# Performance work log

Measured on AMD Instinct MI355X. Metric: run time of the kernel, lower is better.

Reference implementation:

```python
import jax, jax.numpy as jnp
import numpy as np

DIM = 1024
NUM_HEADS = 16
HEAD_DIM = DIM // NUM_HEADS
EPS = 1e-6


def setup_inputs() -> dict:
    key = jax.random.key(0)
    ks = jax.random.split(key, 12)
    B, S = 2, 2048
    scale = 0.02
    # rope angles -> cos/sin of shape [B, S, HEAD_DIM//2]
    inv_freq = 1.0 / (10000.0 ** (jnp.arange(0, HEAD_DIM, 2, dtype=jnp.float32) / HEAD_DIM))
    t = jnp.arange(S, dtype=jnp.float32)
    ang = jnp.einsum('s,d->sd', t, inv_freq)  # [S, HEAD_DIM//2]
    rope_cos = jnp.broadcast_to(jnp.cos(ang)[None], (B, S, HEAD_DIM // 2))
    rope_sin = jnp.broadcast_to(jnp.sin(ang)[None], (B, S, HEAD_DIM // 2))
    return {
        'hidden_states': jax.random.normal(ks[0], (B, S, DIM), dtype=jnp.float32),
        'rope_cos': rope_cos,
        'rope_sin': rope_sin,
        'Wq': jax.random.normal(ks[1], (DIM, DIM), dtype=jnp.float32) * scale,
        'bq': jnp.zeros((DIM,), jnp.float32),
        'Wk': jax.random.normal(ks[2], (DIM, DIM), dtype=jnp.float32) * scale,
        'bk': jnp.zeros((DIM,), jnp.float32),
        'Wv': jax.random.normal(ks[3], (DIM, DIM), dtype=jnp.float32) * scale,
        'bv': jnp.zeros((DIM,), jnp.float32),
        'q_norm_w': jnp.ones((HEAD_DIM,), jnp.float32),
        'k_norm_w': jnp.ones((HEAD_DIM,), jnp.float32),
        'Wo': jax.random.normal(ks[4], (DIM, DIM), dtype=jnp.float32) * scale,
        'bo': jnp.zeros((DIM,), jnp.float32),
    }


def _rms_norm(x, w):
    # FP32 RMSNorm over last dim (head_dim)
    x32 = x.astype(jnp.float32)
    inv = jax.lax.rsqrt(jnp.mean(x32 * x32, axis=-1, keepdims=True) + EPS)
    return (x32 * inv * w).astype(x.dtype)


def _apply_rope(x, cos, sin):
    # x: [B,H,S,D]; cos/sin: [B,S,D//2] -> broadcast over heads
    xr = x[..., 0::2]
    xi = x[..., 1::2]
    c = cos[:, None, :, :]
    s = sin[:, None, :, :]
    out_r = xr * c - xi * s
    out_i = xr * s + xi * c
    return jnp.stack([out_r, out_i], axis=-1).reshape(x.shape)


def reference(hidden_states, rope_cos, rope_sin, Wq, bq, Wk, bk, Wv, bv,
              q_norm_w, k_norm_w, Wo, bo):
    B, S, D = hidden_states.shape
    H, hd = NUM_HEADS, HEAD_DIM

    def proj(x, W, b):
        y = jnp.einsum('bsd,ed->bse', x, W) + b
        return y.reshape(B, S, H, hd).transpose(0, 2, 1, 3)  # [B,H,S,hd]

    q = proj(hidden_states, Wq, bq)
    k = proj(hidden_states, Wk, bk)
    v = proj(hidden_states, Wv, bv)

    q = _apply_rope(_rms_norm(q, q_norm_w), rope_cos, rope_sin)
    k = _apply_rope(_rms_norm(k, k_norm_w), rope_cos, rope_sin)

    scale = 1.0 / jnp.sqrt(jnp.asarray(hd, hidden_states.dtype))
    scores = jnp.einsum('bhqd,bhkd->bhqk', q, k) * scale
    attn = jax.nn.softmax(scores, axis=-1)
    o = jnp.einsum('bhqk,bhkd->bhqd', attn, v)  # [B,H,S,hd]
    o = o.transpose(0, 2, 1, 3).reshape(B, S, D)
    return jnp.einsum('bsd,ed->bse', o, Wo) + bo
```

## Files before the change

### kernel.cpp

```cpp
#include <hip/hip_runtime.h>
#include <math.h>

#define BATCH 2
#define SEQ 2048
#define D_MODEL 1024
#define NHEAD 16
#define HDIM 64
#define MROWS (BATCH * SEQ)
#define KDIM 1024

typedef __attribute__((ext_vector_type(8))) short bf16x8_t;
typedef __attribute__((ext_vector_type(4))) float f32x4_t;

#define KSCALE 0.18033688011112042f

__device__ __forceinline__ unsigned short f2bf(float x) {
    unsigned u = __builtin_bit_cast(unsigned, x);
    u += 0x7fffu + ((u >> 16) & 1u);
    return (unsigned short)(u >> 16);
}
__device__ __forceinline__ float bf2f(unsigned short h) {
    return __builtin_bit_cast(float, (unsigned)h << 16);
}
__device__ __forceinline__ unsigned cvt_pk_bf16(float lo, float hi) {
    unsigned r;
    asm("v_cvt_pk_bf16_f32 %0, %1, %2" : "=v"(r) : "v"(lo), "v"(hi));
    return r;
}
__device__ __forceinline__ float fexp2(float x) {
    float r;
    asm("v_exp_f32 %0, %1" : "=v"(r) : "v"(x));
    return r;
}

__device__ __forceinline__ void gload_lds16(const void* g, void* l) {
    __builtin_amdgcn_global_load_lds(
        (const __attribute__((address_space(1))) unsigned int*)g,
        (__attribute__((address_space(3))) unsigned int*)l, 16, 0, 0);
}

__global__ __launch_bounds__(256, 3) void gemm_qkv_bf16(
    const unsigned short* __restrict__ hbf,
    const unsigned short* __restrict__ wqb, const unsigned short* __restrict__ wkb,
    const unsigned short* __restrict__ wvb,
    const float* __restrict__ bq, const float* __restrict__ bk,
    const float* __restrict__ bv,
    const float* __restrict__ qw, const float* __restrict__ kw,
    const float* __restrict__ cosb, const float* __restrict__ sinb,
    unsigned short* __restrict__ qbf, unsigned short* __restrict__ kbf,
    unsigned short* __restrict__ vbf)
{
    __shared__ unsigned short lds[16384];
    const int bx = blockIdx.x;
    const int mat = bx >> 3;
    const int nc0 = (bx & 7) * 128;
    const int m0 = blockIdx.y * 128;
    const unsigned short* W = mat == 0 ? wqb : mat == 1 ? wkb : wvb;
    const float* bias = mat == 0 ? bq : mat == 1 ? bk : bv;

    const int tid = threadIdx.x;
    const int lane = tid & 63;
    const int w = tid >> 6;
    const int wm = w >> 1, wn = w & 1;
    const int l15 = lane & 15, lg = lane >> 4;
    const int r_in = lane >> 3, slot = lane & 7;

    f32x4_t acc[4][4];
    #pragma unroll
    for (int i = 0; i < 4; ++i)
        #pragma unroll
        for (int j = 0; j < 4; ++j) acc[i][j] = (f32x4_t){0.f, 0.f, 0.f, 0.f};

    const unsigned short* baseA = hbf + (size_t)m0 * KDIM;
    const unsigned short* baseW = W + (size_t)nc0 * KDIM;
    const int xk = (slot ^ r_in) << 3;

    for (int kt = 0; kt < 16; ++kt) {
        const int k = kt * 64;
        __syncthreads();
        #pragma unroll
        for (int cc = 0; cc < 8; ++cc) {
            const int row = ((((cc & 3) << 2) | w) << 3) + r_in;
            const unsigned short* src =
                (cc < 4 ? baseA : baseW) + (size_t)row * KDIM + k + xk;
            gload_lds16(src, &lds[(size_t)((cc << 2) | w) << 9]);
        }
        __syncthreads();

        #pragma unroll
        for (int ks = 0; ks < 2; ++ks) {
            bf16x8_t ah[4], wh[4];
            #pragma unroll
            for (int i = 0; i < 4; ++i) {
                const int r = wm * 64 + i * 16 + l15;
                const int off = r * 64 + ((((ks << 2) | lg) ^ (r & 7)) << 3);
                ah[i] = *(const bf16x8_t*)&lds[off];
            }
            #pragma unroll
            for (int j = 0; j < 4; ++j) {
                const int r = wn * 64 + j * 16 + l15;
                const int off = r * 64 + ((((ks << 2) | lg) ^ (r & 7)) << 3);
                wh[j] = *(const bf16x8_t*)&lds[8192 + off];
            }
            #pragma unroll
            for (int i = 0; i < 4; ++i)
                #pragma unroll
                for (int j = 0; j < 4; ++j)
                    acc[i][j] = __builtin_amdgcn_mfma_f32_16x16x32_bf16(ah[i], wh[j], acc[i][j], 0, 0, 0);
        }
    }

    if (mat == 2) {
        #pragma unroll
        for (int j = 0; j < 4; ++j) {
            const int n = nc0 + wn * 64 + j * 16 + l15;
            const float bb = bias[n];
            #pragma unroll
            for (int i = 0; i < 4; ++i)
                #pragma unroll
                for (int q = 0; q < 4; ++q) {
                    const int m = m0 + wm * 64 + i * 16 + lg * 4 + q;
                    vbf[(size_t)m * D_MODEL + n] = f2bf(acc[i][j][q] + bb);
                }
        }
    } else {
        unsigned short* dst = mat == 0 ? qbf : kbf;
        const float* nw = mat == 0 ? qw : kw;
        float bbj[4], wj[4];
        #pragma unroll
        for (int j = 0; j < 4; ++j) {
            bbj[j] = bias[nc0 + wn * 64 + j * 16 + l15];
            wj[j] = nw[j * 16 + l15];
        }
        const int headn = (nc0 + wn * 64) >> 6;
        #pragma unroll
        for (int i = 0; i < 4; ++i) {
            #pragma unroll
            for (int q = 0; q < 4; ++q) {
                const int m = m0 + wm * 64 + i * 16 + lg * 4 + q;
                float v[4];
                float ss = 0.0f;
                #pragma unroll
                for (int j = 0; j < 4; ++j) {
                    v[j] = acc[i][j][q] + bbj[j];
                    ss = fmaf(v[j], v[j], ss);
                }
                ss += __shfl_xor(ss, 1);
                ss += __shfl_xor(ss, 2);
                ss += __shfl_xor(ss, 4);
                ss += __shfl_xor(ss, 8);
                const float inv = rsqrtf(ss * (1.0f / 64.0f) + 1e-6f);
                const int bh = ((m >> 11) << 4) | headn;
                const size_t rowoff = (((size_t)bh << 11) | (size_t)(m & 2047)) << 6;
                #pragma unroll
                for (int j = 0; j < 4; ++j) {
                    float val = v[j] * inv * wj[j];
                    float partner = __shfl_xor(val, 1);
                    const int d = j * 16 + l15;
                    const float c = cosb[(size_t)m * (HDIM / 2) + (d >> 1)];
                    const float s = sinb[(size_t)m * (HDIM / 2) + (d >> 1)];
                    float outv = (l15 & 1) ? fmaf(partner, s, val * c)
                                           : fmaf(val, c, -partner * s);
                    if (mat) outv *= KSCALE;
                    dst[rowoff | d] = f2bf(outv);
                }
            }
        }
    }
}

__global__ __launch_bounds__(256, 2) void gemm_out(
    const unsigned short* __restrict__ ohi, const unsigned short* __restrict__ olo,
    const unsigned short* __restrict__ woh, const unsigned short* __restrict__ wol,
    const float* __restrict__ bo, float* __restrict__ out)
{
    __shared__ unsigned short lds[24576];
    const int nc0 = blockIdx.x * 64;
    const int m0 = blockIdx.y * 128;

    const int tid = threadIdx.x;
    const int lane = tid & 63;
    const int w = tid >> 6;
    const int l15 = lane & 15, lg = lane >> 4;
    const int r_in = lane >> 3, slot = lane & 7;

    f32x4_t acc[2][4];
    #pragma unroll
    for (int i = 0; i < 2; ++i)
        #pragma unroll
        for (int j = 0; j < 4; ++j) acc[i][j] = (f32x4_t){0.f, 0.f, 0.f, 0.f};

    const unsigned short* bA0 = ohi + (size_t)m0 * KDIM;
    const unsigned short* bA1 = olo + (size_t)m0 * KDIM;
    const unsigned short* bW0 = woh + (size_t)nc0 * KDIM;
    const unsigned short* bW1 = wol + (size_t)nc0 * KDIM;
    const int xk = (slot ^ r_in) << 3;

    for (int kt = 0; kt < 16; ++kt) {
        const int k = kt * 64;
        __syncthreads();
        #pragma unroll
        for (int cc = 0; cc < 12; ++cc) {
            const unsigned short* srcb;
            int row, base;
            if (cc < 4)       { srcb = bA0; row = cc * 32;        base = cc * 2048; }
            else if (cc < 8)  { srcb = bA1; row = (cc - 4) * 32;  base = 8192 + (cc - 4) * 2048; }
            else if (cc < 10) { srcb = bW0; row = (cc - 8) * 32;  base = 16384 + (cc - 8) * 2048; }
            else              { srcb = bW1; row = (cc - 10) * 32; base = 20480 + (cc - 10) * 2048; }
            row += w * 8 + r_in;
            gload_lds16(srcb + (size_t)row * KDIM + k + xk, &lds[base + w * 512]);
        }
        __syncthreads();

        #pragma unroll
        for (int ks = 0; ks < 2; ++ks) {
            bf16x8_t ah[2], al[2], wh[4], wl[4];
            #pragma unroll
            for (int i = 0; i < 2; ++i) {
                const int r = w * 32 + i * 16 + l15;
                const int off = r * 64 + ((((ks << 2) | lg) ^ (r & 7)) << 3);
                ah[i] = *(const bf16x8_t*)&lds[off];
                al[i] = *(const bf16x8_t*)&lds[8192 + off];
            }
            #pragma unroll
            for (int j = 0; j < 4; ++j) {
                const int r = j * 16 + l15;
                const int off = r * 64 + ((((ks << 2) | lg) ^ (r & 7)) << 3);
                wh[j] = *(const bf16x8_t*)&lds[16384 + off];
                wl[j] = *(const bf16x8_t*)&lds[20480 + off];
            }
            #pragma unroll
            for (int i = 0; i < 2; ++i)
                #pragma unroll
                for (int j = 0; j < 4; ++j) {
                    acc[i][j] = __builtin_amdgcn_mfma_f32_16x16x32_bf16(ah[i], wh[j], acc[i][j], 0, 0, 0);
                    acc[i][j] = __builtin_amdgcn_mfma_f32_16x16x32_bf16(ah[i], wl[j], acc[i][j], 0, 0, 0);
                    acc[i][j] = __builtin_amdgcn_mfma_f32_16x16x32_bf16(al[i], wh[j], acc[i][j], 0, 0, 0);
                }
        }
    }

    #pragma unroll
    for (int j = 0; j < 4; ++j) {
        const int n = nc0 + j * 16 + l15;
        const float bb = bo[n];
        #pragma unroll
        for (int i = 0; i < 2; ++i)
            #pragma unroll
            for (int q = 0; q < 4; ++q) {
                const int m = m0 + w * 32 + i * 16 + lg * 4 + q;
                out[(size_t)m * D_MODEL + n] = acc[i][j][q] + bb;
            }
    }
}

__global__ __launch_bounds__(256) void pack_all(
    const float* __restrict__ w0, const float* __restrict__ w1,
    const float* __restrict__ w2, const float* __restrict__ w3,
    const float* __restrict__ hsrc,
    unsigned short* __restrict__ b0, unsigned short* __restrict__ b1,
    unsigned short* __restrict__ b2,
    unsigned short* __restrict__ h3, unsigned short* __restrict__ l3,
    unsigned short* __restrict__ hdst)
{
    const int y = blockIdx.y;
    if (y < 3) {
        const float* src = y == 0 ? w0 : y == 1 ? w1 : w2;
        unsigned short* dst = y == 0 ? b0 : y == 1 ? b1 : b2;
        const int n4 = D_MODEL * D_MODEL / 4;
        for (int i = blockIdx.x * 256 + threadIdx.x; i < n4; i += gridDim.x * 256) {
            float4 v = ((const float4*)src)[i];
            ushort4 h;
            h.x = f2bf(v.x); h.y = f2bf(v.y); h.z = f2bf(v.z); h.w = f2bf(v.w);
            ((ushort4*)dst)[i] = h;
        }
    } else if (y == 3) {
        const int n4 = D_MODEL * D_MODEL / 4;
        for (int i = blockIdx.x * 256 + threadIdx.x; i < n4; i += gridDim.x * 256) {
            float4 v = ((const float4*)w3)[i];
            ushort4 h, l;
            h.x = f2bf(v.x); l.x = f2bf(v.x - bf2f(h.x));
            h.y = f2bf(v.y); l.y = f2bf(v.y - bf2f(h.y));
            h.z = f2bf(v.z); l.z = f2bf(v.z - bf2f(h.z));
            h.w = f2bf(v.w); l.w = f2bf(v.w - bf2f(h.w));
            ((ushort4*)h3)[i] = h;
            ((ushort4*)l3)[i] = l;
        }
    } else {
        const int n4 = MROWS * D_MODEL / 4;
        for (int i = blockIdx.x * 256 + threadIdx.x; i < n4; i += gridDim.x * 256) {
            float4 v = ((const float4*)hsrc)[i];
            ushort4 h;
            h.x = f2bf(v.x); h.y = f2bf(v.y); h.z = f2bf(v.z); h.w = f2bf(v.w);
            ((ushort4*)hdst)[i] = h;
        }
    }
}

__global__ __launch_bounds__(256) void vtrans_bf(
    const unsigned short* __restrict__ vbf, unsigned short* __restrict__ vbt)
{
    __shared__ unsigned short T[64][72];
    const int tid = threadIdx.x;
    const int bh = blockIdx.y;
    const int b = bh >> 4, h = bh & 15;
    const int s0 = blockIdx.x * 64;

    const int sr = tid >> 2;
    const int dc = (tid & 3) << 4;
    const unsigned short* src = vbf + ((size_t)b * SEQ + s0 + sr) * D_MODEL + h * HDIM + dc;
    unsigned short tmp[16];
    *(bf16x8_t*)tmp = *(const bf16x8_t*)src;
    *(bf16x8_t*)(tmp + 8) = *(const bf16x8_t*)(src + 8);
    #pragma unroll
    for (int i = 0; i < 16; ++i) T[dc + i][sr] = tmp[i];
    __syncthreads();

    const int dr = tid >> 2;
    const int sc = (tid & 3) << 4;
    unsigned short ov[16];
    #pragma unroll
    for (int i = 0; i < 16; ++i) ov[i] = T[dr][sc + i];
    unsigned short* dst = vbt + ((size_t)bh * HDIM + dr) * SEQ + s0 + sc;
    *(bf16x8_t*)dst = *(bf16x8_t*)ov;
    *(bf16x8_t*)(dst + 8) = *(bf16x8_t*)(ov + 8);
}

__global__ __launch_bounds__(256, 2) void attn_mfma(
    const unsigned short* __restrict__ qbf,
    const unsigned short* __restrict__ kbf,
    const unsigned short* __restrict__ vbt,
    unsigned short* __restrict__ ohi,
    unsigned short* __restrict__ olo)
{
    __shared__ __align__(16) char slds[49152];

    const int tid = threadIdx.x;
    const int lane = tid & 63;
    const int w = tid >> 6;
    const int l15 = lane & 15;
    const int lg = lane >> 4;
    const int e7 = l15 & 7;

    const int bh = blockIdx.y;
    const int q0 = blockIdx.x * 128;
    const int b = bh >> 4, h = bh & 15;

    bf16x8_t qa[2][2];
    #pragma unroll
    for (int g = 0; g < 2; ++g) {
        const size_t qrow = ((size_t)bh * SEQ + q0 + w * 32 + g * 16 + l15) * HDIM;
        qa[g][0] = *(const bf16x8_t*)&qbf[qrow + lg * 8];
        qa[g][1] = *(const bf16x8_t*)&qbf[qrow + 32 + lg * 8];
    }

    float lsum0 = 0.0f, lsum1 = 0.0f;
    f32x4_t oacc[2][4];
    #pragma unroll
    for (int g = 0; g < 2; ++g)
        #pragma unroll
        for (int db = 0; db < 4; ++db) oacc[g][db] = (f32x4_t){0.f, 0.f, 0.f, 0.f};

    const unsigned short* kt_base = kbf + (size_t)bh * SEQ * HDIM;
    const unsigned short* vt_base = vbt + (size_t)bh * HDIM * SEQ;

    const int lrow = (lane >> 3) & 7;
    const int lch = lane & 7;
    const unsigned short* kg0 = kt_base + (w * 16 + lrow) * HDIM + ((lch ^ lrow) << 3);
    const unsigned short* kg1 = kg0 + 8 * HDIM;
    const unsigned short* vg0 = vt_base + (size_t)(w * 16 + lrow) * SEQ + ((lch ^ lrow) << 3);
    const unsigned short* vg1 = vg0 + (size_t)8 * SEQ;

    char* const sK = slds;
    char* const sV = slds + 16384;
    char* const sP = slds + 32768;
    const int woff = w << 11;

    gload_lds16(kg0, sK + woff);
    gload_lds16(kg1, sK + woff + 1024);
    gload_lds16(vg0, sV + woff);
    gload_lds16(vg1, sV + woff + 1024);
    kg0 += 64 * HDIM; kg1 += 64 * HDIM;
    vg0 += 64; vg1 += 64;

    const f32x4_t cinit = (f32x4_t){-16.f, -16.f, -16.f, -16.f};
    unsigned sel = 0;

    for (int kt = 0; kt < SEQ / 64; ++kt) {
        __syncthreads();

        if (kt < SEQ / 64 - 1) {
            const unsigned nsel = sel ^ 8192;
            gload_lds16(kg0, sK + nsel + woff);
            gload_lds16(kg1, sK + nsel + woff + 1024);
            gload_lds16(vg0, sV + nsel + woff);
            gload_lds16(vg1, sV + nsel + woff + 1024);
            kg0 += 64 * HDIM; kg1 += 64 * HDIM;
            vg0 += 64; vg1 += 64;
        }

        const char* kb_ = sK + sel;
        const char* vb_ = sV + sel;

        f32x4_t sc0[4], sc1[4];
        #pragma unroll
        for (int kb = 0; kb < 4; ++kb) { sc0[kb] = cinit; sc1[kb] = cinit; }
        __builtin_amdgcn_s_setprio(1);
        #pragma unroll
        for (int ks = 0; ks < 2; ++ks) {
            #pragma unroll
            for (int kb = 0; kb < 4; ++kb) {
                bf16x8_t kf = *(const bf16x8_t*)(kb_ + (kb * 16 + l15) * 128
                                 + ((((ks << 2) | lg) ^ e7) << 4));
                sc0[kb] = __builtin_amdgcn_mfma_f32_16x16x32_bf16(kf, qa[0][ks], sc0[kb], 0, 0, 0);
                sc1[kb] = __builtin_amdgcn_mfma_f32_16x16x32_bf16(kf, qa[1][ks], sc1[kb], 0, 0, 0);
            }
        }
        __builtin_amdgcn_s_setprio(0);

        #pragma unroll
        for (int kb = 0; kb < 4; ++kb) {
            const int c = (kb << 1) | (lg >> 1);
            const int slot = ((c ^ e7) << 4) + ((lg & 1) << 3);
            {
                float p0 = fexp2(sc0[kb][0]);
                float p1 = fexp2(sc0[kb][1]);
                float p2 = fexp2(sc0[kb][2]);
                float p3 = fexp2(sc0[kb][3]);
                lsum0 += (p0 + p1) + (p2 + p3);
                uint2 uu;
                uu.x = cvt_pk_bf16(p0, p1);
                uu.y = cvt_pk_bf16(p2, p3);
                *(uint2*)(sP + (w * 32 + l15) * 128 + slot) = uu;
            }
            {
                float p0 = fexp2(sc1[kb][0]);
                float p1 = fexp2(sc1[kb][1]);
                float p2 = fexp2(sc1[kb][2]);
                float p3 = fexp2(sc1[kb][3]);
                lsum1 += (p0 + p1) + (p2 + p3);
                uint2 uu;
                uu.x = cvt_pk_bf16(p0, p1);
                uu.y = cvt_pk_bf16(p2, p3);
                *(uint2*)(sP + (w * 32 + 16 + l15) * 128 + slot) = uu;
            }
        }

        __builtin_amdgcn_s_setprio(1);
        #pragma unroll
        for (int ks = 0; ks < 2; ++ks) {
            const int poff = ((((ks << 2) | lg) ^ e7) << 4);
            bf16x8_t pa0 = *(const bf16x8_t*)(sP + (w * 32 + l15) * 128 + poff);
            bf16x8_t pa1 = *(const bf16x8_t*)(sP + (w * 32 + 16 + l15) * 128 + poff);
            #pragma unroll
            for (int db = 0; db < 4; ++db) {
                bf16x8_t vf = *(const bf16x8_t*)(vb_ + (db * 16 + l15) * 128 + poff);
                oacc[0][db] = __builtin_amdgcn_mfma_f32_16x16x32_bf16(pa0, vf, oacc[0][db], 0, 0, 0);
                oacc[1][db] = __builtin_amdgcn_mfma_f32_16x16x32_bf16(pa1, vf, oacc[1][db], 0, 0, 0);
            }
        }
        __builtin_amdgcn_s_setprio(0);

        sel ^= 8192;
    }

    lsum0 += __shfl_xor(lsum0, 16);
    lsum0 += __shfl_xor(lsum0, 32);
    lsum1 += __shfl_xor(lsum1, 16);
    lsum1 += __shfl_xor(lsum1, 32);
    const float linv0 = 1.0f / lsum0;
    const float linv1 = 1.0f / lsum1;

    #pragma unroll
    for (int g = 0; g < 2; ++g) {
        const float linv = g ? linv1 : linv0;
        #pragma unroll
        for (int r = 0; r < 4; ++r) {
            float lr = __shfl(linv, (lane & 48) | (lg * 4 + r));
            #pragma unroll
            for (int db = 0; db < 4; ++db) {
                size_t oi = ((size_t)b * SEQ + q0 + w * 32 + g * 16 + lg * 4 + r) * D_MODEL
                            + h * HDIM + db * 16 + l15;
                float val = oacc[g][db][r] * lr;
                unsigned short hv = f2bf(val);
                ohi[oi] = hv;
                olo[oi] = f2bf(val - bf2f(hv));
            }
        }
    }
}

extern "C" void kernel_launch(void* const* d_in, const int* in_sizes, int n_in,
                              void* d_out, int out_size, void* d_ws, size_t ws_size,
                              hipStream_t stream)
{
    const float* hidden = (const float*)d_in[0];
    const float* cosb   = (const float*)d_in[1];
    const float* sinb   = (const float*)d_in[2];
    const float* Wq     = (const float*)d_in[3];
    const float* bq     = (const float*)d_in[4];
    const float* Wk     = (const float*)d_in[5];
    const float* bk     = (const float*)d_in[6];
    const float* Wv     = (const float*)d_in[7];
    const float* bv     = (const float*)d_in[8];
    const float* qw     = (const float*)d_in[9];
    const float* kw     = (const float*)d_in[10];
    const float* Wo     = (const float*)d_in[11];
    const float* bo     = (const float*)d_in[12];
    float* out = (float*)d_out;

    char* ws = (char*)d_ws;
    const size_t bsz = (size_t)MROWS * D_MODEL * sizeof(unsigned short);
    const size_t wsz = (size_t)D_MODEL * D_MODEL * sizeof(unsigned short);

    unsigned short* hbf  = (unsigned short*)(ws);
    unsigned short* vbf  = (unsigned short*)(ws + bsz);
    unsigned short* qbf  = (unsigned short*)(ws + 2 * bsz);
    unsigned short* kbf  = (unsigned short*)(ws + 3 * bsz);
    unsigned short* vbtT = (unsigned short*)(ws + 4 * bsz);
    unsigned short* ohi  = (unsigned short*)(ws + 5 * bsz);
    unsigned short* olo  = (unsigned short*)(ws + 6 * bsz);
    char* wbase = ws + 7 * bsz;
    unsigned short* wqb = (unsigned short*)(wbase);
    unsigned short* wkb = (unsigned short*)(wbase + wsz);
    unsigned short* wvb = (unsigned short*)(wbase + 2 * wsz);
    unsigned short* woh = (unsigned short*)(wbase + 3 * wsz);
    unsigned short* wol = (unsigned short*)(wbase + 4 * wsz);

    dim3 blk(256);

    pack_all<<<dim3(512, 5), blk, 0, stream>>>(Wq, Wk, Wv, Wo, hidden,
        wqb, wkb, wvb, woh, wol, hbf);

    gemm_qkv_bf16<<<dim3(24, 32), blk, 0, stream>>>(
        hbf, wqb, wkb, wvb, bq, bk, bv, qw, kw, cosb, sinb, qbf, kbf, vbf);

    vtrans_bf<<<dim3(SEQ / 64, BATCH * NHEAD), blk, 0, stream>>>(vbf, vbtT);

    attn_mfma<<<dim3(SEQ / 128, BATCH * NHEAD), blk, 0, stream>>>(
        qbf, kbf, vbtT, ohi, olo);

    gemm_out<<<dim3(16, 32), blk, 0, stream>>>(ohi, olo, woh, wol, bo, out);
}
```

Baseline: 127.4 us.

## Drop split-bf16 output projection and write V transposed from QKV epilogue

```diff
diff --git a/kernel.cpp b/kernel.cpp
--- a/kernel.cpp
+++ b/kernel.cpp
@@ -48,7 +48,7 @@
     const float* __restrict__ qw, const float* __restrict__ kw,
     const float* __restrict__ cosb, const float* __restrict__ sinb,
     unsigned short* __restrict__ qbf, unsigned short* __restrict__ kbf,
-    unsigned short* __restrict__ vbf)
+    unsigned short* __restrict__ vbt)
 {
     __shared__ unsigned short lds[16384];
     const int bx = blockIdx.x;
@@ -115,13 +115,18 @@
         for (int j = 0; j < 4; ++j) {
             const int n = nc0 + wn * 64 + j * 16 + l15;
             const float bb = bias[n];
-            #pragma unroll
-            for (int i = 0; i < 4; ++i)
+            const int head = n >> 6, d = n & 63;
+            #pragma unroll
+            for (int i = 0; i < 4; ++i) {
+                const int mbase = m0 + wm * 64 + i * 16 + lg * 4;
+                const int b_ = mbase >> 11;
+                const int s_ = mbase & 2047;
+                unsigned short o4[4];
                 #pragma unroll
-                for (int q = 0; q < 4; ++q) {
-                    const int m = m0 + wm * 64 + i * 16 + lg * 4 + q;
-                    vbf[(size_t)m * D_MODEL + n] = f2bf(acc[i][j][q] + bb);
-                }
+                for (int q = 0; q < 4; ++q) o4[q] = f2bf(acc[i][j][q] + bb);
+                *(ushort4*)&vbt[(((size_t)(b_ * NHEAD + head) * HDIM + d) << 11) | s_] =
+                    *(ushort4*)o4;
+            }
         }
     } else {
         unsigned short* dst = mat == 0 ? qbf : kbf;
@@ -169,12 +174,12 @@
     }
 }
 
-__global__ __launch_bounds__(256, 2) void gemm_out(
-    const unsigned short* __restrict__ ohi, const unsigned short* __restrict__ olo,
-    const unsigned short* __restrict__ woh, const unsigned short* __restrict__ wol,
+__global__ __launch_bounds__(256, 3) void gemm_out(
+    const unsigned short* __restrict__ obf,
+    const unsigned short* __restrict__ wob,
     const float* __restrict__ bo, float* __restrict__ out)
 {
-    __shared__ unsigned short lds[24576];
+    __shared__ unsigned short lds[12288];
     const int nc0 = blockIdx.x * 64;
     const int m0 = blockIdx.y * 128;
 
@@ -190,53 +195,50 @@
         #pragma unroll
         for (int j = 0; j < 4; ++j) acc[i][j] = (f32x4_t){0.f, 0.f, 0.f, 0.f};
 
-    const unsigned short* bA0 = ohi + (size_t)m0 * KDIM;
-    const unsigned short* bA1 = olo + (size_t)m0 * KDIM;
-    const unsigned short* bW0 = woh + (size_t)nc0 * KDIM;
-    const unsigned short* bW1 = wol + (size_t)nc0 * KDIM;
+    const unsigned short* baseA = obf + (size_t)m0 * KDIM;
+    const unsigned short* baseW = wob + (size_t)nc0 * KDIM;
     const int xk = (slot ^ r_in) << 3;
 
     for (int kt = 0; kt < 16; ++kt) {
         const int k = kt * 64;
         __syncthreads();
         #pragma unroll
-        for (int cc = 0; cc < 12; ++cc) {
+        for (int cc = 0; cc < 6; ++cc) {
             const unsigned short* srcb;
             int row, base;
-            if (cc < 4)       { srcb = bA0; row = cc * 32;        base = cc * 2048; }
-            else if (cc < 8)  { srcb = bA1; row = (cc - 4) * 32;  base = 8192 + (cc - 4) * 2048; }
-            else if (cc < 10) { srcb = bW0; row = (cc - 8) * 32;  base = 16384 + (cc - 8) * 2048; }
-            else              { srcb = bW1; row = (cc - 10) * 32; base = 20480 + (cc - 10) * 2048; }
-            row += w * 8 + r_in;
-            gload_lds16(srcb + (size_t)row * KDIM + k + xk, &lds[base + w * 512]);
+            if (cc < 4) {
+                srcb = baseA;
+                row = (((cc << 2) | w) << 3) + r_in;
+                base = ((cc << 2) | w) << 9;
+            } else {
+                srcb = baseW;
+                row = ((((cc - 4) << 2) | w) << 3) + r_in;
+                base = 8192 + ((((cc - 4) << 2) | w) << 9);
+            }
+            gload_lds16(srcb + (size_t)row * KDIM + k + xk, &lds[base]);
         }
         __syncthreads();
 
         #pragma unroll
         for (int ks = 0; ks < 2; ++ks) {
-            bf16x8_t ah[2], al[2], wh[4], wl[4];
+            bf16x8_t ah[2], wh[4];
             #pragma unroll
             for (int i = 0; i < 2; ++i) {
                 const int r = w * 32 + i * 16 + l15;
                 const int off = r * 64 + ((((ks << 2) | lg) ^ (r & 7)) << 3);
                 ah[i] = *(const bf16x8_t*)&lds[off];
-                al[i] = *(const bf16x8_t*)&lds[8192 + off];
             }
             #pragma unroll
             for (int j = 0; j < 4; ++j) {
                 const int r = j * 16 + l15;
                 const int off = r * 64 + ((((ks << 2) | lg) ^ (r & 7)) << 3);
-                wh[j] = *(const bf16x8_t*)&lds[16384 + off];
-                wl[j] = *(const bf16x8_t*)&lds[20480 + off];
+                wh[j] = *(const bf16x8_t*)&lds[8192 + off];
             }
             #pragma unroll
             for (int i = 0; i < 2; ++i)
                 #pragma unroll
-                for (int j = 0; j < 4; ++j) {
+                for (int j = 0; j < 4; ++j)
                     acc[i][j] = __builtin_amdgcn_mfma_f32_16x16x32_bf16(ah[i], wh[j], acc[i][j], 0, 0, 0);
-                    acc[i][j] = __builtin_amdgcn_mfma_f32_16x16x32_bf16(ah[i], wl[j], acc[i][j], 0, 0, 0);
-                    acc[i][j] = __builtin_amdgcn_mfma_f32_16x16x32_bf16(al[i], wh[j], acc[i][j], 0, 0, 0);
-                }
         }
     }
 
@@ -259,79 +261,35 @@
     const float* __restrict__ w2, const float* __restrict__ w3,
     const float* __restrict__ hsrc,
     unsigned short* __restrict__ b0, unsigned short* __restrict__ b1,
-    unsigned short* __restrict__ b2,
-    unsigned short* __restrict__ h3, unsigned short* __restrict__ l3,
+    unsigned short* __restrict__ b2, unsigned short* __restrict__ b3,
     unsigned short* __restrict__ hdst)
 {
     const int y = blockIdx.y;
-    if (y < 3) {
-        const float* src = y == 0 ? w0 : y == 1 ? w1 : w2;
-        unsigned short* dst = y == 0 ? b0 : y == 1 ? b1 : b2;
-        const int n4 = D_MODEL * D_MODEL / 4;
-        for (int i = blockIdx.x * 256 + threadIdx.x; i < n4; i += gridDim.x * 256) {
-            float4 v = ((const float4*)src)[i];
-            ushort4 h;
-            h.x = f2bf(v.x); h.y = f2bf(v.y); h.z = f2bf(v.z); h.w = f2bf(v.w);
-            ((ushort4*)dst)[i] = h;
-        }
-    } else if (y == 3) {
-        const int n4 = D_MODEL * D_MODEL / 4;
-        for (int i = blockIdx.x * 256 + threadIdx.x; i < n4; i += gridDim.x * 256) {
-            float4 v = ((const float4*)w3)[i];
-            ushort4 h, l;
-            h.x = f2bf(v.x); l.x = f2bf(v.x - bf2f(h.x));
-            h.y = f2bf(v.y); l.y = f2bf(v.y - bf2f(h.y));
-            h.z = f2bf(v.z); l.z = f2bf(v.z - bf2f(h.z));
-            h.w = f2bf(v.w); l.w = f2bf(v.w - bf2f(h.w));
-            ((ushort4*)h3)[i] = h;
-            ((ushort4*)l3)[i] = l;
-        }
+    const float* src;
+    unsigned short* dst;
+    int n4;
+    if (y < 4) {
+        src = y == 0 ? w0 : y == 1 ? w1 : y == 2 ? w2 : w3;
+        dst = y == 0 ? b0 : y == 1 ? b1 : y == 2 ? b2 : b3;
+        n4 = D_MODEL * D_MODEL / 4;
     } else {
-        const int n4 = MROWS * D_MODEL / 4;
-        for (int i = blockIdx.x * 256 + threadIdx.x; i < n4; i += gridDim.x * 256) {
-            float4 v = ((const float4*)hsrc)[i];
-            ushort4 h;
-            h.x = f2bf(v.x); h.y = f2bf(v.y); h.z = f2bf(v.z); h.w = f2bf(v.w);
-            ((ushort4*)hdst)[i] = h;
-        }
-    }
-}
-
-__global__ __launch_bounds__(256) void vtrans_bf(
-    const unsigned short* __restrict__ vbf, unsigned short* __restrict__ vbt)
-{
-    __shared__ unsigned short T[64][72];
-    const int tid = threadIdx.x;
-    const int bh = blockIdx.y;
-    const int b = bh >> 4, h = bh & 15;
-    const int s0 = blockIdx.x * 64;
-
-    const int sr = tid >> 2;
-    const int dc = (tid & 3) << 4;
-    const unsigned short* src = vbf + ((size_t)b * SEQ + s0 + sr) * D_MODEL + h * HDIM + dc;
-    unsigned short tmp[16];
-    *(bf16x8_t*)tmp = *(const bf16x8_t*)src;
-    *(bf16x8_t*)(tmp + 8) = *(const bf16x8_t*)(src + 8);
-    #pragma unroll
-    for (int i = 0; i < 16; ++i) T[dc + i][sr] = tmp[i];
-    __syncthreads();
-
-    const int dr = tid >> 2;
-    const int sc = (tid & 3) << 4;
-    unsigned short ov[16];
-    #pragma unroll
-    for (int i = 0; i < 16; ++i) ov[i] = T[dr][sc + i];
-    unsigned short* dst = vbt + ((size_t)bh * HDIM + dr) * SEQ + s0 + sc;
-    *(bf16x8_t*)dst = *(bf16x8_t*)ov;
-    *(bf16x8_t*)(dst + 8) = *(bf16x8_t*)(ov + 8);
+        src = hsrc;
+        dst = hdst;
+        n4 = MROWS * D_MODEL / 4;
+    }
+    for (int i = blockIdx.x * 256 + threadIdx.x; i < n4; i += gridDim.x * 256) {
+        float4 v = ((const float4*)src)[i];
+        ushort4 h;
+        h.x = f2bf(v.x); h.y = f2bf(v.y); h.z = f2bf(v.z); h.w = f2bf(v.w);
+        ((ushort4*)dst)[i] = h;
+    }
 }
 
 __global__ __launch_bounds__(256, 2) void attn_mfma(
     const unsigned short* __restrict__ qbf,
     const unsigned short* __restrict__ kbf,
     const unsigned short* __restrict__ vbt,
-    unsigned short* __restrict__ ohi,
-    unsigned short* __restrict__ olo)
+    unsigned short* __restrict__ obf)
 {
     __shared__ __align__(16) char slds[49152];
 
@@ -481,10 +439,7 @@
             for (int db = 0; db < 4; ++db) {
                 size_t oi = ((size_t)b * SEQ + q0 + w * 32 + g * 16 + lg * 4 + r) * D_MODEL
                             + h * HDIM + db * 16 + l15;
-                float val = oacc[g][db][r] * lr;
-                unsigned short hv = f2bf(val);
-                ohi[oi] = hv;
-                olo[oi] = f2bf(val - bf2f(hv));
+                obf[oi] = f2bf(oacc[g][db][r] * lr);
             }
         }
     }
@@ -514,31 +469,26 @@
     const size_t wsz = (size_t)D_MODEL * D_MODEL * sizeof(unsigned short);
 
     unsigned short* hbf  = (unsigned short*)(ws);
-    unsigned short* vbf  = (unsigned short*)(ws + bsz);
-    unsigned short* qbf  = (unsigned short*)(ws + 2 * bsz);
-    unsigned short* kbf  = (unsigned short*)(ws + 3 * bsz);
-    unsigned short* vbtT = (unsigned short*)(ws + 4 * bsz);
-    unsigned short* ohi  = (unsigned short*)(ws + 5 * bsz);
-    unsigned short* olo  = (unsigned short*)(ws + 6 * bsz);
-    char* wbase = ws + 7 * bsz;
+    unsigned short* qbf  = (unsigned short*)(ws + bsz);
+    unsigned short* kbf  = (unsigned short*)(ws + 2 * bsz);
+    unsigned short* vbt  = (unsigned short*)(ws + 3 * bsz);
+    unsigned short* obf  = (unsigned short*)(ws + 4 * bsz);
+    char* wbase = ws + 5 * bsz;
     unsigned short* wqb = (unsigned short*)(wbase);
     unsigned short* wkb = (unsigned short*)(wbase + wsz);
     unsigned short* wvb = (unsigned short*)(wbase + 2 * wsz);
-    unsigned short* woh = (unsigned short*)(wbase + 3 * wsz);
-    unsigned short* wol = (unsigned short*)(wbase + 4 * wsz);
+    unsigned short* wob = (unsigned short*)(wbase + 3 * wsz);
 
     dim3 blk(256);
 
     pack_all<<<dim3(512, 5), blk, 0, stream>>>(Wq, Wk, Wv, Wo, hidden,
-        wqb, wkb, wvb, woh, wol, hbf);
+        wqb, wkb, wvb, wob, hbf);
 
     gemm_qkv_bf16<<<dim3(24, 32), blk, 0, stream>>>(
-        hbf, wqb, wkb, wvb, bq, bk, bv, qw, kw, cosb, sinb, qbf, kbf, vbf);
-
-    vtrans_bf<<<dim3(SEQ / 64, BATCH * NHEAD), blk, 0, stream>>>(vbf, vbtT);
+        hbf, wqb, wkb, wvb, bq, bk, bv, qw, kw, cosb, sinb, qbf, kbf, vbt);
 
     attn_mfma<<<dim3(SEQ / 128, BATCH * NHEAD), blk, 0, stream>>>(
-        qbf, kbf, vbtT, ohi, olo);
-
-    gemm_out<<<dim3(16, 32), blk, 0, stream>>>(ohi, olo, woh, wol, bo, out);
-}
+        qbf, kbf, vbt, obf);
+
+    gemm_out<<<dim3(16, 32), blk, 0, stream>>>(obf, wob, bo, out);
+}
```

Measured after the change: 111.3 us. 12.6% less time.
